# Performance work log

Measured on AMD Instinct MI355X. Metric: run time of the kernel, lower is better.

## Reference

```python
import jax, jax.numpy as jnp
import numpy as np

TOP_K = 2  # cfg.MODEL.MOE.TOP_K


def setup_inputs() -> dict:
    key = jax.random.key(0)
    ks = jax.random.split(key, 5)
    bs, L, d_in, d_out, E = 32, 1024, 768, 256, 8
    return {
        "x": jax.random.normal(ks[0], (bs, L, d_in), dtype=jnp.float32),
        "gate_W": jax.random.normal(ks[1], (d_in, E), dtype=jnp.float32) * (1.0 / np.sqrt(d_in)),
        "gate_b": jax.random.normal(ks[2], (E,), dtype=jnp.float32) * 0.01,
        "expert_W": jax.random.normal(ks[3], (E, d_in, d_out), dtype=jnp.float32) * (1.0 / np.sqrt(d_in)),
        "expert_b": jax.random.normal(ks[4], (E, d_out), dtype=jnp.float32) * 0.01,
    }


def reference(x, gate_W, gate_b, expert_W, expert_b):
    # Gate: (bs, L, E) softmax over experts, then top-k routing weights.
    gate_logits = jnp.einsum("bli,ie->ble", x, gate_W) + gate_b
    gate_weights = jax.nn.softmax(gate_logits, axis=-1)
    topk_vals, topk_idx = jax.lax.top_k(gate_weights, TOP_K)  # (bs, L, K)

    # Dense all-expert projection (E is small), then gather the selected ones.
    # all_out: (bs, L, E, d_out)
    all_out = jnp.einsum("bli,eio->bleo", x, expert_W) + expert_b

    # Select top-k expert outputs per token: (bs, L, K, d_out)
    sel = jnp.take_along_axis(all_out, topk_idx[..., None], axis=2)

    # Weighted combine over the K routed experts -> (bs, L, d_out)
    output = jnp.sum(sel * topk_vals[..., None], axis=2)
    return output
```

## Files before the change

kernel.cpp:

```cpp
#include <hip/hip_runtime.h>
#include <hip/hip_bf16.h>
#include <stdint.h>

#define T_TOKENS 32768
#define D_IN     768
#define D_OUT    256
#define N_EXP    8
#define S_TOT    (T_TOKENS*2)
#define S_PAD    66560
#define KSPLIT   6

typedef __attribute__((ext_vector_type(8))) short bf16x8;
typedef __attribute__((ext_vector_type(4))) float f32x4;

__device__ __forceinline__ unsigned short f2bf(float f) {
    unsigned u = __float_as_uint(f);
    return (unsigned short)((u + 0x7FFFu + ((u >> 16) & 1u)) >> 16);
}
__device__ __forceinline__ unsigned pack_bf2(float a, float b) {
    return (unsigned)f2bf(a) | ((unsigned)f2bf(b) << 16);
}

__device__ __forceinline__ void async16(void* lds, const void* g) {
    __builtin_amdgcn_global_load_lds(
        (const __attribute__((address_space(1))) unsigned int*)g,
        (__attribute__((address_space(3))) unsigned int*)lds, 16, 0, 0);
}

__global__ void convw_kernel(const float* __restrict__ W, unsigned short* __restrict__ WT,
                             int* __restrict__ zero16) {
    if (blockIdx.x == 0 && threadIdx.x < 16) zero16[threadIdx.x] = 0;
    int idx = blockIdx.x * 256 + threadIdx.x;
    float v = W[idx];
    int n  = idx & 255;
    int ek = idx >> 8;
    int k  = ek % D_IN;
    int e  = ek / D_IN;
    WT[(size_t)e * (D_IN * D_OUT) + (size_t)n * D_IN + k] = f2bf(v);
}

__global__ __launch_bounds__(64) void gate_partial_kernel(
        const float* __restrict__ x, const float* __restrict__ gW,
        unsigned short* __restrict__ xbf, float* __restrict__ partial) {
    __shared__ float tile[64 * 65];
    int tid = threadIdx.x;
    int t0  = blockIdx.x * 64;
    int kq  = blockIdx.y;
    int c16 = tid & 15, rb = tid >> 4;
    float acc[8] = {0,0,0,0,0,0,0,0};
    #pragma unroll 1
    for (int j = 0; j < 2; j++) {
        int kc = kq * 128 + j * 64;
        #pragma unroll
        for (int i = 0; i < 16; i++) {
            int row = i * 4 + rb;
            size_t g = (size_t)(t0 + row) * D_IN + kc + c16 * 4;
            float4 v = *(const float4*)(x + g);
            uint2 p; p.x = pack_bf2(v.x, v.y); p.y = pack_bf2(v.z, v.w);
            *(uint2*)(xbf + g) = p;
            float* d = &tile[row * 65 + c16 * 4];
            d[0] = v.x; d[1] = v.y; d[2] = v.z; d[3] = v.w;
        }
        __syncthreads();
        const float* gr = gW + (size_t)kc * 8;
        #pragma unroll 8
        for (int kk = 0; kk < 64; kk++) {
            float xv = tile[tid * 65 + kk];
            #pragma unroll
            for (int e = 0; e < 8; e++) acc[e] += xv * gr[kk * 8 + e];
        }
        __syncthreads();
    }
    float* dst = partial + ((size_t)kq * T_TOKENS + t0 + tid) * 8;
    float4 o0 = {acc[0], acc[1], acc[2], acc[3]};
    float4 o1 = {acc[4], acc[5], acc[6], acc[7]};
    *(float4*)dst = o0; *(float4*)(dst + 4) = o1;
}

__global__ __launch_bounds__(256) void gate_final_kernel(
        const float* __restrict__ partial, const float* __restrict__ gb,
        float* __restrict__ topk_w, int* __restrict__ topk_e, int* __restrict__ counts) {
    __shared__ int h[8];
    int tid = threadIdx.x;
    if (tid < 8) h[tid] = 0;
    __syncthreads();
    int t = blockIdx.x * 256 + tid;
    float acc[8] = {0,0,0,0,0,0,0,0};
    #pragma unroll
    for (int q = 0; q < KSPLIT; q++) {
        const float* p = partial + ((size_t)q * T_TOKENS + t) * 8;
        float4 a = *(const float4*)p;
        float4 b = *(const float4*)(p + 4);
        acc[0] += a.x; acc[1] += a.y; acc[2] += a.z; acc[3] += a.w;
        acc[4] += b.x; acc[5] += b.y; acc[6] += b.z; acc[7] += b.w;
    }
    float mx = -1e30f;
    #pragma unroll
    for (int e = 0; e < 8; e++) { acc[e] += gb[e]; mx = fmaxf(mx, acc[e]); }
    float w[8], s = 0.f;
    #pragma unroll
    for (int e = 0; e < 8; e++) { w[e] = expf(acc[e] - mx); s += w[e]; }
    float inv = 1.0f / s;
    int e0 = 0; float b0 = -1.f;
    #pragma unroll
    for (int e = 0; e < 8; e++) if (w[e] > b0) { b0 = w[e]; e0 = e; }
    int e1 = 0; float b1 = -1.f;
    #pragma unroll
    for (int e = 0; e < 8; e++) if (e != e0 && w[e] > b1) { b1 = w[e]; e1 = e; }
    topk_w[t*2]   = b0 * inv;
    topk_w[t*2+1] = b1 * inv;
    topk_e[t*2]   = e0;
    topk_e[t*2+1] = e1;
    atomicAdd(&h[e0], 1); atomicAdd(&h[e1], 1);
    __syncthreads();
    if (tid < 8) atomicAdd(&counts[tid], h[tid]);
}

__global__ void scatter_kernel(const int* __restrict__ topk_e, const float* __restrict__ topk_w,
                               const int* __restrict__ counts, int* __restrict__ cursors,
                               int* __restrict__ slot_token, float* __restrict__ slot_w,
                               int* __restrict__ inv_slot) {
    int offs[9]; offs[0] = 0;
    #pragma unroll
    for (int e = 0; e < 8; e++) offs[e+1] = offs[e] + ((counts[e] + 127) & ~127);
    __shared__ int hcnt[8], hbase[8];
    if (threadIdx.x < 8) hcnt[threadIdx.x] = 0;
    __syncthreads();
    int idx[4], ee[4], lr[4];
    int base = blockIdx.x * 256 * 4 + threadIdx.x;
    #pragma unroll
    for (int j = 0; j < 4; j++) {
        idx[j] = base + j * 256;
        ee[j]  = topk_e[idx[j]];
        lr[j]  = atomicAdd(&hcnt[ee[j]], 1);
    }
    __syncthreads();
    if (threadIdx.x < 8) hbase[threadIdx.x] = atomicAdd(&cursors[threadIdx.x], hcnt[threadIdx.x]);
    __syncthreads();
    #pragma unroll
    for (int j = 0; j < 4; j++) {
        int slot = offs[ee[j]] + hbase[ee[j]] + lr[j];
        slot_token[slot] = idx[j] >> 1;
        slot_w[slot]     = topk_w[idx[j]];
        inv_slot[idx[j]] = slot;
    }
}

template<bool ROUTED>
__global__ __launch_bounds__(256, 2) void moe_gemm_kernel(
        const unsigned short* __restrict__ xbf, const unsigned short* __restrict__ WT,
        const float* __restrict__ eb, const int* __restrict__ counts,
        const int* __restrict__ slot_token, const float* __restrict__ slot_w,
        float* __restrict__ dst) {
    __shared__ unsigned short A_lds[2][128 * 32];
    __shared__ unsigned short B_lds[2][256 * 32];

    int offs[9]; offs[0] = 0;
    #pragma unroll
    for (int e = 0; e < 8; e++) offs[e+1] = offs[e] + ((counts[e] + 127) & ~127);
    int row0 = blockIdx.x * 128;
    if (row0 >= offs[8]) return;
    int expert = 0;
    #pragma unroll
    for (int e = 0; e < 8; e++) if (row0 >= offs[e]) expert = e;

    int tid  = threadIdx.x;
    int wave = tid >> 6, lane = tid & 63;
    int lrow = lane & 15, lquad = lane >> 4;

    const unsigned short* asrc[2];
    #pragma unroll
    for (int i = 0; i < 2; i++) {
        int c = i * 256 + tid;
        int r = c >> 2, p = c & 3;
        int lc = (p - (r >> 1)) & 3;
        int tok = slot_token[row0 + r];
        tok = tok < 0 ? 0 : (tok >= T_TOKENS ? 0 : tok);
        asrc[i] = xbf + (size_t)tok * D_IN + lc * 8;
    }
    const unsigned short* bb = WT + (size_t)expert * (D_IN * D_OUT);
    const unsigned short* bsrc[4];
    #pragma unroll
    for (int i = 0; i < 4; i++) {
        int c = i * 256 + tid;
        int r = c >> 2, p = c & 3;
        int lc = (p - (r >> 1)) & 3;
        bsrc[i] = bb + (size_t)r * D_IN + lc * 8;
    }

    int a_off[8], b_off[4];
    #pragma unroll
    for (int m = 0; m < 8; m++) {
        int r = m * 16 + lrow;
        a_off[m] = r * 32 + ((lquad + (r >> 1)) & 3) * 8;
    }
    #pragma unroll
    for (int q = 0; q < 4; q++) {
        int r = wave * 64 + q * 16 + lrow;
        b_off[q] = r * 32 + ((lquad + (r >> 1)) & 3) * 8;
    }

    f32x4 acc[8][4];
    #pragma unroll
    for (int m = 0; m < 8; m++)
        #pragma unroll
        for (int q = 0; q < 4; q++) acc[m][q] = (f32x4){0,0,0,0};

    auto stage = [&](int k0, int p) {
        #pragma unroll
        for (int i = 0; i < 2; i++) async16(&A_lds[p][(i * 256 + tid) * 8], asrc[i] + k0);
        #pragma unroll
        for (int i = 0; i < 4; i++) async16(&B_lds[p][(i * 256 + tid) * 8], bsrc[i] + k0);
    };

    stage(0, 0);
    #pragma unroll 1
    for (int s = 0; s < D_IN / 32; s++) {
        __syncthreads();
        if (s < D_IN / 32 - 1) stage((s + 1) * 32, (s + 1) & 1);
        int p = s & 1;
        bf16x8 a[8];
        #pragma unroll
        for (int m = 0; m < 8; m++) a[m] = *(const bf16x8*)&A_lds[p][a_off[m]];
        #pragma unroll
        for (int q = 0; q < 4; q++) {
            bf16x8 b = *(const bf16x8*)&B_lds[p][b_off[q]];
            #pragma unroll
            for (int m = 0; m < 8; m++)
                acc[m][q] = __builtin_amdgcn_mfma_f32_16x16x32_bf16(a[m], b, acc[m][q], 0, 0, 0);
        }
    }

    float bias_q[4];
    #pragma unroll
    for (int q = 0; q < 4; q++) bias_q[q] = eb[expert * D_OUT + wave * 64 + q * 16 + lrow];
    #pragma unroll
    for (int m = 0; m < 8; m++) {
        #pragma unroll
        for (int r = 0; r < 4; r++) {
            int slot = row0 + m * 16 + lquad * 4 + r;
            if constexpr (ROUTED) {
                float* drow = dst + (size_t)slot * D_OUT + wave * 64;
                #pragma unroll
                for (int q = 0; q < 4; q++)
                    drow[q * 16 + lrow] = acc[m][q][r] + bias_q[q];
            } else {
                int tk = slot_token[slot];
                float wgt = slot_w[slot];
                #pragma unroll
                for (int q = 0; q < 4; q++)
                    atomicAdd(dst + (size_t)tk * D_OUT + wave * 64 + q * 16 + lrow,
                              wgt * (acc[m][q][r] + bias_q[q]));
            }
        }
    }
}

__global__ void combine_kernel(const float* __restrict__ routed, const int* __restrict__ inv_slot,
                               const float* __restrict__ topk_w, float* __restrict__ out) {
    int flat = blockIdx.x * 256 + threadIdx.x;
    int t = flat >> 6, c = (flat & 63) * 4;
    int   s0 = inv_slot[t*2], s1 = inv_slot[t*2+1];
    float w0 = topk_w[t*2],   w1 = topk_w[t*2+1];
    float4 r0 = *(const float4*)(routed + (size_t)s0 * D_OUT + c);
    float4 r1 = *(const float4*)(routed + (size_t)s1 * D_OUT + c);
    float4 o;
    o.x = w0*r0.x + w1*r1.x; o.y = w0*r0.y + w1*r1.y;
    o.z = w0*r0.z + w1*r1.z; o.w = w0*r0.w + w1*r1.w;
    *(float4*)(out + (size_t)t * D_OUT + c) = o;
}

extern "C" void kernel_launch(void* const* d_in, const int* in_sizes, int n_in,
                              void* d_out, int out_size, void* d_ws, size_t ws_size,
                              hipStream_t stream) {
    const float* x  = (const float*)d_in[0];
    const float* gW = (const float*)d_in[1];
    const float* gb = (const float*)d_in[2];
    const float* eW = (const float*)d_in[3];
    const float* eb = (const float*)d_in[4];
    float* out = (float*)d_out;
    char* ws = (char*)d_ws;

    float* topk_w      = (float*)(ws + 0);
    int*   topk_e      = (int*)  (ws + 262144);
    int*   counts      = (int*)  (ws + 524288);
    int*   cursors     = (int*)  (ws + 524320);
    int*   slot_token  = (int*)  (ws + 524416);
    float* slot_w      = (float*)(ws + 790656);
    int*   inv_slot    = (int*)  (ws + 1056896);
    float* partial     = (float*)(ws + 1319040);
    unsigned short* WT = (unsigned short*)(ws + 7610496);
    unsigned short* xbf= (unsigned short*)(ws + 10756224);
    float* routed      = (float*)(ws + 61087872);
    const size_t NEED_ROUTED = 61087872 + (size_t)S_PAD * D_OUT * 4;
    bool use_routed = (ws_size >= NEED_ROUTED);

    convw_kernel       <<<N_EXP * D_IN * D_OUT / 256, 256, 0, stream>>>(eW, WT, counts);
    gate_partial_kernel<<<dim3(T_TOKENS / 64, KSPLIT), 64, 0, stream>>>(x, gW, xbf, partial);
    gate_final_kernel  <<<T_TOKENS / 256, 256, 0, stream>>>(partial, gb, topk_w, topk_e, counts);
    scatter_kernel     <<<S_TOT / (256 * 4), 256, 0, stream>>>(topk_e, topk_w, counts, cursors,
                                                               slot_token, slot_w, inv_slot);
    if (use_routed) {
        moe_gemm_kernel<true><<<S_PAD / 128, 256, 0, stream>>>(xbf, WT, eb, counts,
                                                               slot_token, slot_w, routed);
        combine_kernel<<<T_TOKENS * D_OUT / 4 / 256, 256, 0, stream>>>(routed, inv_slot,
                                                                       topk_w, out);
    } else {
        hipMemsetAsync(slot_token, 0, 532480, stream);
        hipMemsetAsync(out, 0, (size_t)out_size * sizeof(float), stream);
        moe_gemm_kernel<false><<<S_PAD / 128, 256, 0, stream>>>(xbf, WT, eb, counts,
                                                                slot_token, slot_w, out);
    }
}
```

Baseline: 271.7 us.

## Triple-buffer MoE GEMM K-loop and pre-block expert weights per K-chunk

The expert weights are now converted into a K-blocked bf16 layout, where each 32-wide K chunk for all 256 outputs is contiguous, so each B-tile stage reads one contiguous 16 KB block. The conversion kernel also reads coalesced rows and writes packed words instead of scattered 2-byte stores. The GEMM main loop moves from a double-buffered __syncthreads pipeline to a three-stage ring with explicit vmcnt waits and raw s_barrier, so two tiles are in flight while one is computed. LDS use per block grows by half, which may limit occupancy at two blocks per CU.

New measurement: 269.9 us. About the same (-0.7%).

```diff
diff --git a/kernel.cpp b/kernel.cpp
--- a/kernel.cpp
+++ b/kernel.cpp
@@ -9,6 +9,7 @@
 #define S_TOT    (T_TOKENS*2)
 #define S_PAD    66560
 #define KSPLIT   6
+#define NKB      24
 
 typedef __attribute__((ext_vector_type(8))) short bf16x8;
 typedef __attribute__((ext_vector_type(4))) float f32x4;
@@ -27,16 +28,20 @@
         (__attribute__((address_space(3))) unsigned int*)lds, 16, 0, 0);
 }
 
-__global__ void convw_kernel(const float* __restrict__ W, unsigned short* __restrict__ WT,
-                             int* __restrict__ zero16) {
+__global__ __launch_bounds__(256) void convw_kernel(
+        const float* __restrict__ W, unsigned short* __restrict__ WTb,
+        int* __restrict__ zero16) {
     if (blockIdx.x == 0 && threadIdx.x < 16) zero16[threadIdx.x] = 0;
-    int idx = blockIdx.x * 256 + threadIdx.x;
-    float v = W[idx];
-    int n  = idx & 255;
-    int ek = idx >> 8;
-    int k  = ek % D_IN;
-    int e  = ek / D_IN;
-    WT[(size_t)e * (D_IN * D_OUT) + (size_t)n * D_IN + k] = f2bf(v);
+    int eb_ = blockIdx.x;
+    int n = threadIdx.x;
+    const float* src = W + ((size_t)(eb_ / NKB) * D_IN + (eb_ % NKB) * 32) * 256 + n;
+    unsigned pk[16];
+    #pragma unroll
+    for (int j = 0; j < 16; j++)
+        pk[j] = pack_bf2(src[(2*j) * 256], src[(2*j+1) * 256]);
+    unsigned* dst = (unsigned*)(WTb + ((size_t)eb_ * 256 + n) * 32);
+    #pragma unroll
+    for (int j = 0; j < 16; j++) dst[j] = pk[j];
 }
 
 __global__ __launch_bounds__(64) void gate_partial_kernel(
@@ -148,12 +153,12 @@
 
 template<bool ROUTED>
 __global__ __launch_bounds__(256, 2) void moe_gemm_kernel(
-        const unsigned short* __restrict__ xbf, const unsigned short* __restrict__ WT,
+        const unsigned short* __restrict__ xbf, const unsigned short* __restrict__ WTb,
         const float* __restrict__ eb, const int* __restrict__ counts,
         const int* __restrict__ slot_token, const float* __restrict__ slot_w,
         float* __restrict__ dst) {
-    __shared__ unsigned short A_lds[2][128 * 32];
-    __shared__ unsigned short B_lds[2][256 * 32];
+    __shared__ unsigned short A_lds[3][128 * 32];
+    __shared__ unsigned short B_lds[3][256 * 32];
 
     int offs[9]; offs[0] = 0;
     #pragma unroll
@@ -175,17 +180,17 @@
         int r = c >> 2, p = c & 3;
         int lc = (p - (r >> 1)) & 3;
         int tok = slot_token[row0 + r];
-        tok = tok < 0 ? 0 : (tok >= T_TOKENS ? 0 : tok);
+        tok = (tok < 0 || tok >= T_TOKENS) ? 0 : tok;
         asrc[i] = xbf + (size_t)tok * D_IN + lc * 8;
     }
-    const unsigned short* bb = WT + (size_t)expert * (D_IN * D_OUT);
-    const unsigned short* bsrc[4];
+    const unsigned short* bexp = WTb + (size_t)expert * NKB * 8192;
+    int boff[4];
     #pragma unroll
     for (int i = 0; i < 4; i++) {
         int c = i * 256 + tid;
         int r = c >> 2, p = c & 3;
         int lc = (p - (r >> 1)) & 3;
-        bsrc[i] = bb + (size_t)r * D_IN + lc * 8;
+        boff[i] = r * 32 + lc * 8;
     }
 
     int a_off[8], b_off[4];
@@ -206,19 +211,24 @@
         #pragma unroll
         for (int q = 0; q < 4; q++) acc[m][q] = (f32x4){0,0,0,0};
 
-    auto stage = [&](int k0, int p) {
-        #pragma unroll
-        for (int i = 0; i < 2; i++) async16(&A_lds[p][(i * 256 + tid) * 8], asrc[i] + k0);
-        #pragma unroll
-        for (int i = 0; i < 4; i++) async16(&B_lds[p][(i * 256 + tid) * 8], bsrc[i] + k0);
+    auto stage = [&](int kb, int st) {
+        #pragma unroll
+        for (int i = 0; i < 2; i++)
+            async16(&A_lds[st][(i * 256 + tid) * 8], asrc[i] + kb * 32);
+        const unsigned short* tb = bexp + (size_t)kb * 8192;
+        #pragma unroll
+        for (int i = 0; i < 4; i++)
+            async16(&B_lds[st][(i * 256 + tid) * 8], tb + boff[i]);
     };
 
     stage(0, 0);
-    #pragma unroll 1
-    for (int s = 0; s < D_IN / 32; s++) {
-        __syncthreads();
-        if (s < D_IN / 32 - 1) stage((s + 1) * 32, (s + 1) & 1);
-        int p = s & 1;
+    stage(1, 1);
+    for (int s = 0; s < NKB; s++) {
+        if (s == NKB - 1) asm volatile("s_waitcnt vmcnt(0)" ::: "memory");
+        else              asm volatile("s_waitcnt vmcnt(6)" ::: "memory");
+        asm volatile("s_barrier" ::: "memory");
+        if (s + 2 < NKB) stage(s + 2, (s + 2) % 3);
+        int p = s % 3;
         bf16x8 a[8];
         #pragma unroll
         for (int m = 0; m < 8; m++) a[m] = *(const bf16x8*)&A_lds[p][a_off[m]];
@@ -289,26 +299,26 @@
     float* slot_w      = (float*)(ws + 790656);
     int*   inv_slot    = (int*)  (ws + 1056896);
     float* partial     = (float*)(ws + 1319040);
-    unsigned short* WT = (unsigned short*)(ws + 7610496);
+    unsigned short* WTb= (unsigned short*)(ws + 7610496);
     unsigned short* xbf= (unsigned short*)(ws + 10756224);
     float* routed      = (float*)(ws + 61087872);
     const size_t NEED_ROUTED = 61087872 + (size_t)S_PAD * D_OUT * 4;
     bool use_routed = (ws_size >= NEED_ROUTED);
 
-    convw_kernel       <<<N_EXP * D_IN * D_OUT / 256, 256, 0, stream>>>(eW, WT, counts);
+    convw_kernel       <<<N_EXP * NKB, 256, 0, stream>>>(eW, WTb, counts);
     gate_partial_kernel<<<dim3(T_TOKENS / 64, KSPLIT), 64, 0, stream>>>(x, gW, xbf, partial);
     gate_final_kernel  <<<T_TOKENS / 256, 256, 0, stream>>>(partial, gb, topk_w, topk_e, counts);
     scatter_kernel     <<<S_TOT / (256 * 4), 256, 0, stream>>>(topk_e, topk_w, counts, cursors,
                                                                slot_token, slot_w, inv_slot);
     if (use_routed) {
-        moe_gemm_kernel<true><<<S_PAD / 128, 256, 0, stream>>>(xbf, WT, eb, counts,
+        moe_gemm_kernel<true><<<S_PAD / 128, 256, 0, stream>>>(xbf, WTb, eb, counts,
                                                                slot_token, slot_w, routed);
         combine_kernel<<<T_TOKENS * D_OUT / 4 / 256, 256, 0, stream>>>(routed, inv_slot,
                                                                        topk_w, out);
     } else {
         hipMemsetAsync(slot_token, 0, 532480, stream);
         hipMemsetAsync(out, 0, (size_t)out_size * sizeof(float), stream);
-        moe_gemm_kernel<false><<<S_PAD / 128, 256, 0, stream>>>(xbf, WT, eb, counts,
+        moe_gemm_kernel<false><<<S_PAD / 128, 256, 0, stream>>>(xbf, WTb, eb, counts,
                                                                 slot_token, slot_w, out);
     }
 }
```
